# Kernel optimization log

Measured on AMD Instinct MI355X. Metric: run time of the kernel, lower is better.

The kernel has to match this reference:

```python
import jax, jax.numpy as jnp
import numpy as np

B, N, F, H, L = 8, 4096, 240, 32, 240


def setup_inputs() -> dict:
    key = jax.random.key(0)
    k_x, k_a, k_w1, k_w2 = jax.random.split(key, 4)
    x = jax.random.normal(k_x, (B, N, F), dtype=jnp.float32)
    a = jax.random.uniform(k_a, (N, N), dtype=jnp.float32)
    W1 = jax.random.normal(k_w1, (F, H), dtype=jnp.float32) * (1.0 / np.sqrt(F))
    b1 = jnp.zeros((H,), dtype=jnp.float32)
    W2 = jax.random.normal(k_w2, (H, L), dtype=jnp.float32) * (1.0 / np.sqrt(H))
    b2 = jnp.zeros((L,), dtype=jnp.float32)
    return {"x": x, "a": a, "W1": W1, "b1": b1, "W2": W2, "b2": b2}


def reference(x, a, W1, b1, W2, b2):
    # GCNConv: transform features first (cheap), then aggregate over graph.
    h = jnp.einsum('bnf,fh->bnh', x, W1)            # [B, N, H]
    h = jnp.einsum('nm,bmh->bnh', a, h) + b1        # adjacency aggregation
    h = jax.nn.relu(h)
    # Dense linear head to label dim
    out = jnp.einsum('bnh,hl->bnl', h, W2) + b2     # [B, N, L]
    return out
```

## Files before the change

### kernel.cpp

```cpp
#include <hip/hip_runtime.h>
#include <hip/hip_bf16.h>

#define B_ 8
#define N_ 4096
#define F_ 240
#define H_ 32
#define L_ 240
#define C_ 256
#define KS 4

typedef __attribute__((ext_vector_type(8))) short bf16x8;
typedef __attribute__((ext_vector_type(4))) short bf16x4;
typedef __attribute__((ext_vector_type(4))) float f32x4;

__device__ __forceinline__ short f2bf(float f) {
    union { float f; unsigned u; } v; v.f = f;
    unsigned r = (v.u + 0x7FFFu + ((v.u >> 16) & 1u)) >> 16;
    return (short)r;
}

__global__ __launch_bounds__(256) void stage1(const float* __restrict__ x,
                                              const float* __restrict__ W1,
                                              short* __restrict__ HcT) {
    __shared__ short w1t[32][264];
    __shared__ short xt[64][264];
    const int tid = threadIdx.x;
    const int b  = blockIdx.x >> 6;
    const int m0 = (blockIdx.x & 63) << 6;

    for (int idx = tid; idx < 240 * 32; idx += 256) {
        int f = idx >> 5, h = idx & 31;
        w1t[h][f] = f2bf(W1[idx]);
    }
    for (int idx = tid; idx < 32 * 16; idx += 256) {
        int h = idx >> 4, f = 240 + (idx & 15);
        w1t[h][f] = 0;
    }
    const float* xb = x + ((long)b * N_ + m0) * F_;
    for (int idx = tid; idx < 64 * 60; idx += 256) {
        int row = idx / 60, c4 = idx % 60;
        float4 v = *(const float4*)(xb + row * F_ + c4 * 4);
        bf16x4 s; s.x = f2bf(v.x); s.y = f2bf(v.y); s.z = f2bf(v.z); s.w = f2bf(v.w);
        *(bf16x4*)&xt[row][c4 * 4] = s;
    }
    for (int idx = tid; idx < 64 * 4; idx += 256) {
        int row = idx >> 2, f = 240 + (idx & 3) * 4;
        bf16x4 z = {0, 0, 0, 0};
        *(bf16x4*)&xt[row][f] = z;
    }
    __syncthreads();

    const int w = tid >> 6, lane = tid & 63, q = lane >> 4, r = lane & 15;
    f32x4 acc0 = {0,0,0,0}, acc1 = {0,0,0,0};
#pragma unroll
    for (int kk = 0; kk < 8; ++kk) {
        bf16x8 bfr = *(const bf16x8*)&xt[w * 16 + r][kk * 32 + q * 8];
        bf16x8 a0  = *(const bf16x8*)&w1t[r][kk * 32 + q * 8];
        bf16x8 a1  = *(const bf16x8*)&w1t[16 + r][kk * 32 + q * 8];
        acc0 = __builtin_amdgcn_mfma_f32_16x16x32_bf16(a0, bfr, acc0, 0, 0, 0);
        acc1 = __builtin_amdgcn_mfma_f32_16x16x32_bf16(a1, bfr, acc1, 0, 0, 0);
    }
    const int m = m0 + w * 16 + r;
#pragma unroll
    for (int reg = 0; reg < 4; ++reg) {
        int h0 = q * 4 + reg;
        HcT[(b * 32 + h0) * N_ + m]      = f2bf(acc0[reg]);
        HcT[(b * 32 + 16 + h0) * N_ + m] = f2bf(acc1[reg]);
    }
}

template <bool ATOMIC>
__global__ __launch_bounds__(256) void stage2(const float* __restrict__ a,
                                              const short* __restrict__ HcT,
                                              float* __restrict__ P) {
    __shared__ short als[32][40];
    __shared__ short hls[256][40];
    const int tid = threadIdx.x;
    const int bm = blockIdx.x >> 2;
    const int ks = blockIdx.x & 3;
    const int m0 = bm << 5;
    const int k0 = ks << 10;

    const int w = tid >> 6, lane = tid & 63, q = lane >> 4, r = lane & 15;

    f32x4 acc[2][4];
#pragma unroll
    for (int i = 0; i < 2; ++i)
#pragma unroll
        for (int j = 0; j < 4; ++j) acc[i][j] = (f32x4){0, 0, 0, 0};

    const int arow = tid >> 3, acol = (tid & 7) * 4;

    for (int t = 0; t < 32; ++t) {
        const int k = k0 + t * 32;
        __syncthreads();
        {
            float4 v = *(const float4*)(a + (long)(m0 + arow) * N_ + k + acol);
            bf16x4 s; s.x = f2bf(v.x); s.y = f2bf(v.y); s.z = f2bf(v.z); s.w = f2bf(v.w);
            *(bf16x4*)&als[arow][acol] = s;
        }
#pragma unroll
        for (int i = 0; i < 4; ++i) {
            int idx = tid + i * 256;
            int c = idx >> 2, kb = idx & 3;
            bf16x8 v = *(const bf16x8*)(HcT + (long)c * N_ + k + kb * 8);
            *(bf16x8*)&hls[c][kb * 8] = v;
        }
        __syncthreads();
#pragma unroll
        for (int i = 0; i < 2; ++i) {
            bf16x8 af = *(const bf16x8*)&als[i * 16 + r][q * 8];
#pragma unroll
            for (int j = 0; j < 4; ++j) {
                bf16x8 bfr = *(const bf16x8*)&hls[w * 64 + j * 16 + r][q * 8];
                acc[i][j] = __builtin_amdgcn_mfma_f32_16x16x32_bf16(af, bfr, acc[i][j], 0, 0, 0);
            }
        }
    }
#pragma unroll
    for (int i = 0; i < 2; ++i)
#pragma unroll
        for (int j = 0; j < 4; ++j) {
            int c = w * 64 + j * 16 + r;
#pragma unroll
            for (int reg = 0; reg < 4; ++reg) {
                int m = m0 + i * 16 + q * 4 + reg;
                if (ATOMIC) atomicAdd(&P[(long)m * C_ + c], acc[i][j][reg]);
                else        P[((long)ks * N_ + m) * C_ + c] = acc[i][j][reg];
            }
        }
}

__global__ __launch_bounds__(256) void stage3(const float* __restrict__ P,
                                              const float* __restrict__ b1,
                                              const float* __restrict__ W2,
                                              const float* __restrict__ b2,
                                              float* __restrict__ out,
                                              int nks) {
    __shared__ float h2[64][32];
    const int tid = threadIdx.x;
    const int g0 = blockIdx.x * 64;
    const int b  = g0 >> 12;
    const int n0 = g0 & 4095;

    for (int idx = tid; idx < 64 * 32; idx += 256) {
        int rr = idx >> 5, h = idx & 31;
        long base = (long)(n0 + rr) * C_ + b * 32 + h;
        float v = b1[h];
        for (int ks = 0; ks < nks; ++ks) v += P[(long)ks * (N_ * C_) + base];
        h2[rr][h] = v > 0.f ? v : 0.f;
    }
    __syncthreads();

    if (tid < 240) {
        const int l = tid;
        float w2r[32];
#pragma unroll
        for (int h = 0; h < 32; ++h) w2r[h] = W2[h * 240 + l];
        const float bias = b2[l];
        for (int rr = 0; rr < 64; ++rr) {
            const f32x4* hv = (const f32x4*)h2[rr];
            float acc = bias;
#pragma unroll
            for (int hh = 0; hh < 8; ++hh) {
                f32x4 v = hv[hh];
                acc += v[0] * w2r[hh * 4 + 0];
                acc += v[1] * w2r[hh * 4 + 1];
                acc += v[2] * w2r[hh * 4 + 2];
                acc += v[3] * w2r[hh * 4 + 3];
            }
            out[(long)(g0 + rr) * 240 + l] = acc;
        }
    }
}

extern "C" void kernel_launch(void* const* d_in, const int* in_sizes, int n_in,
                              void* d_out, int out_size, void* d_ws, size_t ws_size,
                              hipStream_t stream) {
    const float* x  = (const float*)d_in[0];
    const float* a  = (const float*)d_in[1];
    const float* W1 = (const float*)d_in[2];
    const float* b1 = (const float*)d_in[3];
    const float* W2 = (const float*)d_in[4];
    const float* b2 = (const float*)d_in[5];
    float* out = (float*)d_out;

    short* HcT = (short*)d_ws;
    float* P   = (float*)((char*)d_ws + (size_t)C_ * N_ * 2);
    const size_t need = (size_t)C_ * N_ * 2 + (size_t)KS * N_ * C_ * 4;

    stage1<<<512, 256, 0, stream>>>(x, W1, HcT);
    if (ws_size >= need) {
        stage2<false><<<512, 256, 0, stream>>>(a, HcT, P);
        stage3<<<512, 256, 0, stream>>>(P, b1, W2, b2, out, KS);
    } else {
        hipMemsetAsync(P, 0, (size_t)N_ * C_ * 4, stream);
        stage2<true><<<512, 256, 0, stream>>>(a, HcT, P);
        stage3<<<512, 256, 0, stream>>>(P, b1, W2, b2, out, 1);
    }
}
```

Baseline: 198.3 us.

## Store H in MFMA-fragment layout and double-buffer the adjacency GEMM with register prefetch

```diff
diff --git a/kernel.cpp b/kernel.cpp
--- a/kernel.cpp
+++ b/kernel.cpp
@@ -7,7 +7,8 @@
 #define H_ 32
 #define L_ 240
 #define C_ 256
-#define KS 4
+#define KS 8
+#define MT 64
 
 typedef __attribute__((ext_vector_type(8))) short bf16x8;
 typedef __attribute__((ext_vector_type(4))) short bf16x4;
@@ -19,9 +20,14 @@
     return (short)r;
 }
 
+__device__ __forceinline__ long hcf_sidx(int c, int m) {
+    return ((long)(((((m >> 6) * 16 + (c >> 4)) * 2 + ((m >> 5) & 1)) * 64)
+                   + ((m >> 3) & 3) * 16 + (c & 15))) * 8 + (m & 7);
+}
+
 __global__ __launch_bounds__(256) void stage1(const float* __restrict__ x,
                                               const float* __restrict__ W1,
-                                              short* __restrict__ HcT) {
+                                              short* __restrict__ HcF) {
     __shared__ short w1t[32][264];
     __shared__ short xt[64][264];
     const int tid = threadIdx.x;
@@ -64,71 +70,115 @@
 #pragma unroll
     for (int reg = 0; reg < 4; ++reg) {
         int h0 = q * 4 + reg;
-        HcT[(b * 32 + h0) * N_ + m]      = f2bf(acc0[reg]);
-        HcT[(b * 32 + 16 + h0) * N_ + m] = f2bf(acc1[reg]);
+        HcF[hcf_sidx(b * 32 + h0, m)]      = f2bf(acc0[reg]);
+        HcF[hcf_sidx(b * 32 + 16 + h0, m)] = f2bf(acc1[reg]);
     }
 }
 
 template <bool ATOMIC>
-__global__ __launch_bounds__(256) void stage2(const float* __restrict__ a,
-                                              const short* __restrict__ HcT,
-                                              float* __restrict__ P) {
-    __shared__ short als[32][40];
-    __shared__ short hls[256][40];
+__global__ __launch_bounds__(256, 2) void stage2(const float* __restrict__ a,
+                                                 const short* __restrict__ HcF,
+                                                 float* __restrict__ P) {
+    __shared__ short als[2][512 * 8];
     const int tid = threadIdx.x;
-    const int bm = blockIdx.x >> 2;
-    const int ks = blockIdx.x & 3;
-    const int m0 = bm << 5;
-    const int k0 = ks << 10;
+    const int bm = blockIdx.x >> 3;
+    const int ks = blockIdx.x & 7;
+    const int m0 = bm * MT;
+    const int kb0 = ks * 8;
 
     const int w = tid >> 6, lane = tid & 63, q = lane >> 4, r = lane & 15;
-
-    f32x4 acc[2][4];
-#pragma unroll
-    for (int i = 0; i < 2; ++i)
+    const bf16x8* __restrict__ Hv = (const bf16x8*)HcF;
+
+    f32x4 acc[4][4];
+#pragma unroll
+    for (int i = 0; i < 4; ++i)
 #pragma unroll
         for (int j = 0; j < 4; ++j) acc[i][j] = (f32x4){0, 0, 0, 0};
 
-    const int arow = tid >> 3, acol = (tid & 7) * 4;
-
-    for (int t = 0; t < 32; ++t) {
-        const int k = k0 + t * 32;
+    float pre[16];
+    const int f0i  = tid >> 7,        f1i  = (tid + 256) >> 7;
+    const int f0kp = (tid >> 6) & 1,  f1kp = ((tid + 256) >> 6) & 1;
+    const int f0q  = (tid >> 4) & 3,  f0r = tid & 15;
+
+#define LOAD_A(kb)                                                             \
+    {                                                                          \
+        const float* s0 = a + (long)(m0 + f0i * 16 + f0r) * N_                 \
+                            + (kb) * 64 + f0kp * 32 + f0q * 8;                 \
+        const float* s1 = a + (long)(m0 + f1i * 16 + f0r) * N_                 \
+                            + (kb) * 64 + f1kp * 32 + f0q * 8;                 \
+        float4 v0 = *(const float4*)s0, v1 = *(const float4*)(s0 + 4);         \
+        float4 v2 = *(const float4*)s1, v3 = *(const float4*)(s1 + 4);         \
+        pre[0]=v0.x; pre[1]=v0.y; pre[2]=v0.z; pre[3]=v0.w;                    \
+        pre[4]=v1.x; pre[5]=v1.y; pre[6]=v1.z; pre[7]=v1.w;                    \
+        pre[8]=v2.x; pre[9]=v2.y; pre[10]=v2.z; pre[11]=v2.w;                  \
+        pre[12]=v3.x; pre[13]=v3.y; pre[14]=v3.z; pre[15]=v3.w;                \
+    }
+#define STORE_A(buf)                                                           \
+    {                                                                          \
+        bf16x8 s0, s1;                                                         \
+        _Pragma("unroll") for (int e = 0; e < 8; ++e) {                        \
+            s0[e] = f2bf(pre[e]); s1[e] = f2bf(pre[8 + e]);                    \
+        }                                                                      \
+        *(bf16x8*)&als[buf][tid * 8]         = s0;                             \
+        *(bf16x8*)&als[buf][(tid + 256) * 8] = s1;                             \
+    }
+
+    LOAD_A(kb0);
+    STORE_A(0);
+
+    bf16x8 bcur[8];
+#pragma unroll
+    for (int kp = 0; kp < 2; ++kp)
+#pragma unroll
+        for (int j = 0; j < 4; ++j)
+            bcur[kp * 4 + j] = Hv[(long)((kb0 * 16 + w * 4 + j) * 2 + kp) * 64 + lane];
+
+    __syncthreads();
+
+    for (int t = 0; t < 8; ++t) {
+        const int cur = t & 1;
+        bf16x8 bnxt[8];
+        if (t < 7) {
+            LOAD_A(kb0 + t + 1);
+#pragma unroll
+            for (int kp = 0; kp < 2; ++kp)
+#pragma unroll
+                for (int j = 0; j < 4; ++j)
+                    bnxt[kp * 4 + j] =
+                        Hv[(long)(((kb0 + t + 1) * 16 + w * 4 + j) * 2 + kp) * 64 + lane];
+        }
+#pragma unroll
+        for (int kp = 0; kp < 2; ++kp)
+#pragma unroll
+            for (int i = 0; i < 4; ++i) {
+                bf16x8 af = *(const bf16x8*)&als[cur][((i * 2 + kp) * 64 + lane) * 8];
+#pragma unroll
+                for (int j = 0; j < 4; ++j)
+                    acc[i][j] = __builtin_amdgcn_mfma_f32_16x16x32_bf16(
+                        af, bcur[kp * 4 + j], acc[i][j], 0, 0, 0);
+            }
+        if (t < 7) {
+            STORE_A(!cur);
+#pragma unroll
+            for (int u = 0; u < 8; ++u) bcur[u] = bnxt[u];
+        }
         __syncthreads();
-        {
-            float4 v = *(const float4*)(a + (long)(m0 + arow) * N_ + k + acol);
-            bf16x4 s; s.x = f2bf(v.x); s.y = f2bf(v.y); s.z = f2bf(v.z); s.w = f2bf(v.w);
-            *(bf16x4*)&als[arow][acol] = s;
-        }
-#pragma unroll
-        for (int i = 0; i < 4; ++i) {
-            int idx = tid + i * 256;
-            int c = idx >> 2, kb = idx & 3;
-            bf16x8 v = *(const bf16x8*)(HcT + (long)c * N_ + k + kb * 8);
-            *(bf16x8*)&hls[c][kb * 8] = v;
-        }
-        __syncthreads();
-#pragma unroll
-        for (int i = 0; i < 2; ++i) {
-            bf16x8 af = *(const bf16x8*)&als[i * 16 + r][q * 8];
-#pragma unroll
-            for (int j = 0; j < 4; ++j) {
-                bf16x8 bfr = *(const bf16x8*)&hls[w * 64 + j * 16 + r][q * 8];
-                acc[i][j] = __builtin_amdgcn_mfma_f32_16x16x32_bf16(af, bfr, acc[i][j], 0, 0, 0);
-            }
-        }
-    }
-#pragma unroll
-    for (int i = 0; i < 2; ++i)
+    }
+
+#pragma unroll
+    for (int i = 0; i < 4; ++i)
 #pragma unroll
         for (int j = 0; j < 4; ++j) {
-            int c = w * 64 + j * 16 + r;
+            const int c = w * 64 + j * 16 + r;
 #pragma unroll
             for (int reg = 0; reg < 4; ++reg) {
-                int m = m0 + i * 16 + q * 4 + reg;
+                const int m = m0 + i * 16 + q * 4 + reg;
                 if (ATOMIC) atomicAdd(&P[(long)m * C_ + c], acc[i][j][reg]);
                 else        P[((long)ks * N_ + m) * C_ + c] = acc[i][j][reg];
             }
         }
+#undef LOAD_A
+#undef STORE_A
 }
 
 __global__ __launch_bounds__(256) void stage3(const float* __restrict__ P,
@@ -137,18 +187,23 @@
                                               const float* __restrict__ b2,
                                               float* __restrict__ out,
                                               int nks) {
-    __shared__ float h2[64][32];
+    __shared__ float h2[32][36];
     const int tid = threadIdx.x;
-    const int g0 = blockIdx.x * 64;
+    const int g0 = blockIdx.x * 32;
     const int b  = g0 >> 12;
     const int n0 = g0 & 4095;
 
-    for (int idx = tid; idx < 64 * 32; idx += 256) {
-        int rr = idx >> 5, h = idx & 31;
-        long base = (long)(n0 + rr) * C_ + b * 32 + h;
-        float v = b1[h];
-        for (int ks = 0; ks < nks; ++ks) v += P[(long)ks * (N_ * C_) + base];
-        h2[rr][h] = v > 0.f ? v : 0.f;
+    {
+        const int rr = tid >> 3, c4 = tid & 7;
+        const float* base = P + (long)(n0 + rr) * C_ + b * 32 + c4 * 4;
+        f32x4 s = *(const f32x4*)base;
+        for (int ks = 1; ks < nks; ++ks)
+            s += *(const f32x4*)(base + (long)ks * (N_ * C_));
+        s += *(const f32x4*)(b1 + c4 * 4);
+        f32x4 z;
+#pragma unroll
+        for (int e = 0; e < 4; ++e) z[e] = s[e] > 0.f ? s[e] : 0.f;
+        *(f32x4*)&h2[rr][c4 * 4] = z;
     }
     __syncthreads();
 
@@ -158,7 +213,7 @@
 #pragma unroll
         for (int h = 0; h < 32; ++h) w2r[h] = W2[h * 240 + l];
         const float bias = b2[l];
-        for (int rr = 0; rr < 64; ++rr) {
+        for (int rr = 0; rr < 32; ++rr) {
             const f32x4* hv = (const f32x4*)h2[rr];
             float acc = bias;
 #pragma unroll
@@ -185,17 +240,17 @@
     const float* b2 = (const float*)d_in[5];
     float* out = (float*)d_out;
 
-    short* HcT = (short*)d_ws;
+    short* HcF = (short*)d_ws;
     float* P   = (float*)((char*)d_ws + (size_t)C_ * N_ * 2);
     const size_t need = (size_t)C_ * N_ * 2 + (size_t)KS * N_ * C_ * 4;
 
-    stage1<<<512, 256, 0, stream>>>(x, W1, HcT);
+    stage1<<<512, 256, 0, stream>>>(x, W1, HcF);
     if (ws_size >= need) {
-        stage2<false><<<512, 256, 0, stream>>>(a, HcT, P);
-        stage3<<<512, 256, 0, stream>>>(P, b1, W2, b2, out, KS);
+        stage2<false><<<512, 256, 0, stream>>>(a, HcF, P);
+        stage3<<<1024, 256, 0, stream>>>(P, b1, W2, b2, out, KS);
     } else {
         hipMemsetAsync(P, 0, (size_t)N_ * C_ * 4, stream);
-        stage2<true><<<512, 256, 0, stream>>>(a, HcT, P);
-        stage3<<<512, 256, 0, stream>>>(P, b1, W2, b2, out, 1);
-    }
-}
+        stage2<true><<<512, 256, 0, stream>>>(a, HcF, P);
+        stage3<<<1024, 256, 0, stream>>>(P, b1, W2, b2, out, 1);
+    }
+}
```

After: 171.4 us. 1.16x faster.
